# Performance work log

Measured on AMD Instinct MI355X. Metric: run time of the kernel, lower is better.

## Reference

```python
import jax, jax.numpy as jnp
import numpy as np

B, T, I, E, K, J = 4, 4096, 512, 16, 1024, 512

def setup_inputs() -> dict:
    key = jax.random.key(0)
    k1, k2, k3 = jax.random.split(key, 3)
    X = jax.random.normal(k1, (B, T, I), dtype=jnp.float32)
    ind = jax.random.randint(k2, (B, E, K), 0, T, dtype=jnp.int64)
    W = jax.random.normal(k3, (E, I, J), dtype=jnp.float32)
    return {"X": X, "ind": ind, "W": W}

def reference(X, ind, W):
    # X: [B,T,I], ind: [B,E,K] indices into T (per batch), W: [E,I,J]
    b, t, i = X.shape
    offset = (jnp.arange(b, dtype=ind.dtype) * t)[:, None, None]  # [B,1,1]
    X_flat = X.reshape(b * t, i)
    gathered = X_flat[ind + offset]              # [B,E,K,I]
    Y = jnp.einsum('beki,eij->bekj', gathered, W)  # [B,E,K,J]
    return Y
```

## Files before the change

kernel.cpp:

```cpp
#include <hip/hip_runtime.h>

#define B_ 4
#define T_ 4096
#define I_ 512
#define E_ 16
#define K_ 1024
#define J_ 512

typedef unsigned short u16;
typedef __attribute__((ext_vector_type(4))) float floatx4;
typedef __attribute__((ext_vector_type(8))) short short8;
typedef __attribute__((ext_vector_type(4))) u16 u16x4;
typedef __attribute__((ext_vector_type(8))) u16 u16x8;

__device__ __forceinline__ u16 f2bf(float f) {
  unsigned int u = __float_as_uint(f);
  u += 0x7FFFu + ((u >> 16) & 1u);
  return (u16)(u >> 16);
}

__device__ __forceinline__ void gload16(const u16* g, u16* l) {
  __builtin_amdgcn_global_load_lds(
      (const __attribute__((address_space(1))) unsigned int*)(g),
      (__attribute__((address_space(3))) unsigned int*)(l),
      16, 0, 0);
}

__global__ __launch_bounds__(256) void cvt_x(const float* __restrict__ X,
                                             u16* __restrict__ Xb) {
  const int n4 = B_ * T_ * I_ / 4;
  int i = blockIdx.x * 256 + threadIdx.x;
  const int stride = gridDim.x * 256;
  for (; i < n4; i += stride) {
    floatx4 v = ((const floatx4*)X)[i];
    u16x4 o;
    o[0] = f2bf(v[0]); o[1] = f2bf(v[1]); o[2] = f2bf(v[2]); o[3] = f2bf(v[3]);
    ((u16x4*)Xb)[i] = o;
  }
}

__global__ __launch_bounds__(256) void transp_w(const float* __restrict__ W,
                                                u16* __restrict__ Wt) {
  __shared__ u16 tile[64][65];
  const int tid = threadIdx.x;
  const int blk = blockIdx.x;
  const int e  = blk >> 6;
  const int bi = (blk >> 3) & 7;
  const int bj = blk & 7;
  const int i0 = bi * 64, j0 = bj * 64;

#pragma unroll
  for (int p = 0; p < 4; ++p) {
    int r = p * 16 + (tid >> 4);
    int c = (tid & 15) * 4;
    floatx4 v = *(const floatx4*)(W + ((size_t)(e * I_ + i0 + r)) * J_ + j0 + c);
    tile[r][c + 0] = f2bf(v[0]);
    tile[r][c + 1] = f2bf(v[1]);
    tile[r][c + 2] = f2bf(v[2]);
    tile[r][c + 3] = f2bf(v[3]);
  }
  __syncthreads();
#pragma unroll
  for (int p = 0; p < 2; ++p) {
    int j = p * 32 + (tid >> 3);
    int ch = tid & 7;
    u16x8 o;
#pragma unroll
    for (int s = 0; s < 8; ++s) o[s] = tile[ch * 8 + s][j];
    *(u16x8*)(Wt + ((size_t)(e * J_ + j0 + j)) * I_ + i0 + ch * 8) = o;
  }
}

__global__ __launch_bounds__(256) void gemm_gather(const u16* __restrict__ Xb,
                                                   const u16* __restrict__ Wt,
                                                   const int* __restrict__ ind,
                                                   float* __restrict__ Y) {
  __shared__ alignas(16) u16 Asf[128 * 64];
  __shared__ alignas(16) u16 Bsf[128 * 64];

  const int tid = threadIdx.x;
  const int blk = blockIdx.x;
  const int n_t = blk & 3;
  const int m_t = (blk >> 2) & 7;
  const int be  = blk >> 5;
  const int e = be & 15;
  const int b = be >> 4;

  const int lane = tid & 63;
  const int wave = tid >> 6;

  const int lr = lane >> 3;
  const int cg = (lane & 7) ^ lr;

  const u16* agp[4];
  const u16* bgp[4];
  u16* aldst[4];
  u16* bldst[4];
#pragma unroll
  for (int q = 0; q < 4; ++q) {
    const int r = wave * 32 + q * 8 + lr;
    const int t = ind[be * K_ + m_t * 128 + r];
    agp[q] = Xb + ((size_t)(b * T_ + t)) * I_ + cg * 8;
    bgp[q] = Wt + ((size_t)(e * J_ + n_t * 128 + r)) * I_ + cg * 8;
    aldst[q] = Asf + (wave * 32 + q * 8) * 64;
    bldst[q] = Bsf + (wave * 32 + q * 8) * 64;
  }

  const int wj = (wave & 1) * 64;
  const int wk = (wave >> 1) * 64;
  const int ml = lane & 15;
  const int quad = lane >> 4;

  floatx4 acc[4][4] = {};

  for (int kk = 0; kk < I_; kk += 64) {
#pragma unroll
    for (int q = 0; q < 4; ++q) gload16(agp[q] + kk, aldst[q]);
#pragma unroll
    for (int q = 0; q < 4; ++q) gload16(bgp[q] + kk, bldst[q]);
    __syncthreads();
#pragma unroll
    for (int s = 0; s < 2; ++s) {
      short8 wf[4], xf[4];
      const int c = s * 4 + quad;
#pragma unroll
      for (int i = 0; i < 4; ++i) {
        const int jr = wj + i * 16 + ml;
        const int kr = wk + i * 16 + ml;
        wf[i] = *(const short8*)&Bsf[jr * 64 + ((c ^ (jr & 7)) * 8)];
        xf[i] = *(const short8*)&Asf[kr * 64 + ((c ^ (kr & 7)) * 8)];
      }
#pragma unroll
      for (int iw = 0; iw < 4; ++iw)
#pragma unroll
        for (int ik = 0; ik < 4; ++ik)
          acc[iw][ik] = __builtin_amdgcn_mfma_f32_16x16x32_bf16(
              wf[iw], xf[ik], acc[iw][ik], 0, 0, 0);
    }
    __syncthreads();
  }

#pragma unroll
  for (int iw = 0; iw < 4; ++iw) {
    const int j0 = n_t * 128 + wj + iw * 16 + quad * 4;
#pragma unroll
    for (int ik = 0; ik < 4; ++ik) {
      const int k0 = m_t * 128 + wk + ik * 16 + ml;
      *(floatx4*)(Y + ((size_t)(be * K_ + k0)) * J_ + j0) = acc[iw][ik];
    }
  }
}

extern "C" void kernel_launch(void* const* d_in, const int* in_sizes, int n_in,
                              void* d_out, int out_size, void* d_ws,
                              size_t ws_size, hipStream_t stream) {
  const float* X  = (const float*)d_in[0];
  const int* ind  = (const int*)d_in[1];
  const float* W  = (const float*)d_in[2];
  float* Y = (float*)d_out;

  u16* Xb = (u16*)d_ws;
  u16* Wt = (u16*)((char*)d_ws + (size_t)B_ * T_ * I_ * 2);

  cvt_x<<<2048, 256, 0, stream>>>(X, Xb);
  transp_w<<<1024, 256, 0, stream>>>(W, Wt);
  gemm_gather<<<2048, 256, 0, stream>>>(Xb, Wt, ind, Y);
}
```

Measured before the change: 215.5 us.

## Enlarge GEMM M tile to 256 and merge prep kernels into one launch

Each GEMM block now computes a 256x128 output tile instead of 128x128, halving the grid and doubling per-wave accumulators to 4x8 MFMA tiles. The goal is more reuse of the W fragments and fewer redundant W loads per output. The X conversion and W transpose kernels are merged into one launch to save a launch gap. Gather offsets are held as 32-bit values to save registers. The larger accumulator set raises register pressure under launch_bounds(256,2), and fewer blocks reduce parallelism.

```diff
diff --git a/kernel.cpp b/kernel.cpp
--- a/kernel.cpp
+++ b/kernel.cpp
@@ -8,6 +8,7 @@
 #define J_ 512
 
 typedef unsigned short u16;
+typedef unsigned int u32;
 typedef __attribute__((ext_vector_type(4))) float floatx4;
 typedef __attribute__((ext_vector_type(8))) short short8;
 typedef __attribute__((ext_vector_type(4))) u16 u16x4;
@@ -26,63 +27,62 @@
       16, 0, 0);
 }
 
-__global__ __launch_bounds__(256) void cvt_x(const float* __restrict__ X,
-                                             u16* __restrict__ Xb) {
-  const int n4 = B_ * T_ * I_ / 4;
-  int i = blockIdx.x * 256 + threadIdx.x;
-  const int stride = gridDim.x * 256;
-  for (; i < n4; i += stride) {
-    floatx4 v = ((const floatx4*)X)[i];
-    u16x4 o;
-    o[0] = f2bf(v[0]); o[1] = f2bf(v[1]); o[2] = f2bf(v[2]); o[3] = f2bf(v[3]);
-    ((u16x4*)Xb)[i] = o;
+__global__ __launch_bounds__(256) void prep(const float* __restrict__ X,
+                                            const float* __restrict__ W,
+                                            u16* __restrict__ Xb,
+                                            u16* __restrict__ Wt) {
+  const int tid = threadIdx.x;
+  const int blk = blockIdx.x;
+  if (blk < 1024) {
+    __shared__ u16 tile[64][65];
+    const int e  = blk >> 6;
+    const int bi = (blk >> 3) & 7;
+    const int bj = blk & 7;
+    const int i0 = bi * 64, j0 = bj * 64;
+#pragma unroll
+    for (int p = 0; p < 4; ++p) {
+      int r = p * 16 + (tid >> 4);
+      int c = (tid & 15) * 4;
+      floatx4 v = *(const floatx4*)(W + ((size_t)(e * I_ + i0 + r)) * J_ + j0 + c);
+      tile[r][c + 0] = f2bf(v[0]);
+      tile[r][c + 1] = f2bf(v[1]);
+      tile[r][c + 2] = f2bf(v[2]);
+      tile[r][c + 3] = f2bf(v[3]);
+    }
+    __syncthreads();
+#pragma unroll
+    for (int p = 0; p < 2; ++p) {
+      int j = p * 32 + (tid >> 3);
+      int ch = tid & 7;
+      u16x8 o;
+#pragma unroll
+      for (int s = 0; s < 8; ++s) o[s] = tile[ch * 8 + s][j];
+      *(u16x8*)(Wt + ((size_t)(e * J_ + j0 + j)) * I_ + i0 + ch * 8) = o;
+    }
+  } else {
+    const int n4 = B_ * T_ * I_ / 4;
+    int i = (blk - 1024) * 256 + tid;
+    const int stride = 2048 * 256;
+    for (; i < n4; i += stride) {
+      floatx4 v = ((const floatx4*)X)[i];
+      u16x4 o;
+      o[0] = f2bf(v[0]); o[1] = f2bf(v[1]); o[2] = f2bf(v[2]); o[3] = f2bf(v[3]);
+      ((u16x4*)Xb)[i] = o;
+    }
   }
 }
 
-__global__ __launch_bounds__(256) void transp_w(const float* __restrict__ W,
-                                                u16* __restrict__ Wt) {
-  __shared__ u16 tile[64][65];
-  const int tid = threadIdx.x;
-  const int blk = blockIdx.x;
-  const int e  = blk >> 6;
-  const int bi = (blk >> 3) & 7;
-  const int bj = blk & 7;
-  const int i0 = bi * 64, j0 = bj * 64;
-
-#pragma unroll
-  for (int p = 0; p < 4; ++p) {
-    int r = p * 16 + (tid >> 4);
-    int c = (tid & 15) * 4;
-    floatx4 v = *(const floatx4*)(W + ((size_t)(e * I_ + i0 + r)) * J_ + j0 + c);
-    tile[r][c + 0] = f2bf(v[0]);
-    tile[r][c + 1] = f2bf(v[1]);
-    tile[r][c + 2] = f2bf(v[2]);
-    tile[r][c + 3] = f2bf(v[3]);
-  }
-  __syncthreads();
-#pragma unroll
-  for (int p = 0; p < 2; ++p) {
-    int j = p * 32 + (tid >> 3);
-    int ch = tid & 7;
-    u16x8 o;
-#pragma unroll
-    for (int s = 0; s < 8; ++s) o[s] = tile[ch * 8 + s][j];
-    *(u16x8*)(Wt + ((size_t)(e * J_ + j0 + j)) * I_ + i0 + ch * 8) = o;
-  }
-}
-
-__global__ __launch_bounds__(256) void gemm_gather(const u16* __restrict__ Xb,
-                                                   const u16* __restrict__ Wt,
-                                                   const int* __restrict__ ind,
-                                                   float* __restrict__ Y) {
-  __shared__ alignas(16) u16 Asf[128 * 64];
+__global__ __launch_bounds__(256, 2) void gemm_gather(
+    const u16* __restrict__ Xb, const u16* __restrict__ Wt,
+    const int* __restrict__ ind, float* __restrict__ Y) {
+  __shared__ alignas(16) u16 Asf[256 * 64];
   __shared__ alignas(16) u16 Bsf[128 * 64];
 
   const int tid = threadIdx.x;
   const int blk = blockIdx.x;
-  const int n_t = blk & 3;
-  const int m_t = (blk >> 2) & 7;
-  const int be  = blk >> 5;
+  const int m_t = blk & 3;
+  const int n_t = (blk >> 2) & 3;
+  const int be  = blk >> 4;
   const int e = be & 15;
   const int b = be >> 4;
 
@@ -92,50 +92,49 @@
   const int lr = lane >> 3;
   const int cg = (lane & 7) ^ lr;
 
-  const u16* agp[4];
-  const u16* bgp[4];
-  u16* aldst[4];
-  u16* bldst[4];
+  u32 aoff[8];
 #pragma unroll
-  for (int q = 0; q < 4; ++q) {
-    const int r = wave * 32 + q * 8 + lr;
-    const int t = ind[be * K_ + m_t * 128 + r];
-    agp[q] = Xb + ((size_t)(b * T_ + t)) * I_ + cg * 8;
-    bgp[q] = Wt + ((size_t)(e * J_ + n_t * 128 + r)) * I_ + cg * 8;
-    aldst[q] = Asf + (wave * 32 + q * 8) * 64;
-    bldst[q] = Bsf + (wave * 32 + q * 8) * 64;
+  for (int q = 0; q < 8; ++q) {
+    const int r = wave * 64 + q * 8 + lr;
+    const int t = ind[be * K_ + m_t * 256 + r];
+    aoff[q] = (u32)(b * T_ + t) * I_ + cg * 8;
   }
+  const u16* bbase =
+      Wt + ((size_t)(e * J_ + n_t * 128 + wave * 32 + lr)) * I_ + cg * 8;
+  u16* ald = Asf + (wave * 64) * 64;
+  u16* bld = Bsf + (wave * 32) * 64;
 
   const int wj = (wave & 1) * 64;
-  const int wk = (wave >> 1) * 64;
+  const int wk = (wave >> 1) * 128;
   const int ml = lane & 15;
   const int quad = lane >> 4;
 
-  floatx4 acc[4][4] = {};
+  floatx4 acc[4][8] = {};
 
   for (int kk = 0; kk < I_; kk += 64) {
 #pragma unroll
-    for (int q = 0; q < 4; ++q) gload16(agp[q] + kk, aldst[q]);
+    for (int q = 0; q < 8; ++q) gload16(Xb + aoff[q] + kk, ald + q * 512);
 #pragma unroll
-    for (int q = 0; q < 4; ++q) gload16(bgp[q] + kk, bldst[q]);
+    for (int q = 0; q < 4; ++q) gload16(bbase + q * 8 * I_ + kk, bld + q * 512);
     __syncthreads();
 #pragma unroll
     for (int s = 0; s < 2; ++s) {
-      short8 wf[4], xf[4];
       const int c = s * 4 + quad;
+      short8 wf[4];
 #pragma unroll
       for (int i = 0; i < 4; ++i) {
         const int jr = wj + i * 16 + ml;
-        const int kr = wk + i * 16 + ml;
         wf[i] = *(const short8*)&Bsf[jr * 64 + ((c ^ (jr & 7)) * 8)];
-        xf[i] = *(const short8*)&Asf[kr * 64 + ((c ^ (kr & 7)) * 8)];
       }
 #pragma unroll
-      for (int iw = 0; iw < 4; ++iw)
+      for (int ik = 0; ik < 8; ++ik) {
+        const int kr = wk + ik * 16 + ml;
+        const short8 xf = *(const short8*)&Asf[kr * 64 + ((c ^ (kr & 7)) * 8)];
 #pragma unroll
-        for (int ik = 0; ik < 4; ++ik)
+        for (int iw = 0; iw < 4; ++iw)
           acc[iw][ik] = __builtin_amdgcn_mfma_f32_16x16x32_bf16(
-              wf[iw], xf[ik], acc[iw][ik], 0, 0, 0);
+              wf[iw], xf, acc[iw][ik], 0, 0, 0);
+      }
     }
     __syncthreads();
   }
@@ -144,8 +143,8 @@
   for (int iw = 0; iw < 4; ++iw) {
     const int j0 = n_t * 128 + wj + iw * 16 + quad * 4;
 #pragma unroll
-    for (int ik = 0; ik < 4; ++ik) {
-      const int k0 = m_t * 128 + wk + ik * 16 + ml;
+    for (int ik = 0; ik < 8; ++ik) {
+      const int k0 = m_t * 256 + wk + ik * 16 + ml;
       *(floatx4*)(Y + ((size_t)(be * K_ + k0)) * J_ + j0) = acc[iw][ik];
     }
   }
@@ -162,7 +161,6 @@
   u16* Xb = (u16*)d_ws;
   u16* Wt = (u16*)((char*)d_ws + (size_t)B_ * T_ * I_ * 2);
 
-  cvt_x<<<2048, 256, 0, stream>>>(X, Xb);
-  transp_w<<<1024, 256, 0, stream>>>(W, Wt);
-  gemm_gather<<<2048, 256, 0, stream>>>(Xb, Wt, ind, Y);
+  prep<<<3072, 256, 0, stream>>>(X, W, Xb, Wt);
+  gemm_gather<<<1024, 256, 0, stream>>>(Xb, Wt, ind, Y);
 }
```

After: 209.9 us. 1.03x faster.
